# Performance work log

Measured on AMD Instinct MI355X. Metric: run time of the kernel, lower is better.

## Reference

```python
import jax, jax.numpy as jnp
import numpy as np

D = 64       # hidden_dim
ED = 16      # edge_dim
N = 50000
E = 400000
T = 2
STEP = 0.5   # euler fixed step over t in [0,1] -> 2 steps
EPS = 1e-5

def setup_inputs() -> dict:
    key = jax.random.key(0)
    ks = jax.random.split(key, 14)
    def lin(k, fi, fo):
        return jax.random.normal(k, (fi, fo), jnp.float32) / np.sqrt(fi)
    return {
        'h_seq': jax.random.normal(ks[0], (T, N, D), jnp.float32),
        'edge_attr': jax.random.normal(ks[1], (T, E, ED), jnp.float32),
        # msg_net: MLP(2D+ED -> D -> D), 2 layers with ReLU
        'W1': lin(ks[2], 2 * D + ED, D), 'b1': jnp.zeros((D,), jnp.float32),
        'W2': lin(ks[3], D, D),          'b2': jnp.zeros((D,), jnp.float32),
        # dynamics_net: Linear(2D,D) -> LayerNorm -> SiLU -> Linear(D,D) -> Tanh
        'Wd1': lin(ks[4], 2 * D, D), 'bd1': jnp.zeros((D,), jnp.float32),
        'ln_g': jnp.ones((D,), jnp.float32), 'ln_b': jnp.zeros((D,), jnp.float32),
        'Wd2': lin(ks[5], D, D), 'bd2': jnp.zeros((D,), jnp.float32),
        'edge_index': jax.random.randint(ks[6], (T, 2, E), 0, N, jnp.int32),
    }

def _ode_func(h, row, col, ea, W1, b1, W2, b2, Wd1, bd1, ln_g, ln_b, Wd2, bd2):
    # identity transport: Q_uv @ h_v == h_v
    h_transported = h[col]                              # [E, D]
    msg_in = jnp.concatenate([h[row], h_transported, ea], axis=-1)  # [E, 2D+ED]
    msg = jax.nn.relu(msg_in @ W1 + b1) @ W2 + b2       # [E, D]
    agg = jax.ops.segment_sum(msg, row, num_segments=h.shape[0])    # [N, D]
    x = jnp.concatenate([h, agg], axis=-1) @ Wd1 + bd1  # [N, D]
    mu = x.mean(-1, keepdims=True)
    var = x.var(-1, keepdims=True)
    x = (x - mu) * jax.lax.rsqrt(var + EPS) * ln_g + ln_b
    x = jax.nn.silu(x) @ Wd2 + bd2
    return jnp.tanh(x)

def reference(h_seq, edge_attr, W1, b1, W2, b2, Wd1, bd1, ln_g, ln_b, Wd2, bd2, edge_index):
    params = (W1, b1, W2, b2, Wd1, bd1, ln_g, ln_b, Wd2, bd2)
    n_steps = int(round(1.0 / STEP))
    h_prev = h_seq[0]
    disagreements = []
    for t in range(T):
        row, col = edge_index[t, 0], edge_index[t, 1]
        ea = edge_attr[t]
        h = h_prev + h_seq[t]                           # h_fused
        for _ in range(n_steps):                        # fixed-step Euler
            h = h + STEP * _ode_func(h, row, col, ea, *params)
        diff = h[row] - h[col]                          # Q=I -> h_u - h_v
        disagreements.append(jnp.minimum((diff * diff).sum(-1), 1e4))
        h_prev = h
    return h_prev, jnp.stack(disagreements)             # h_final [N,D], D [T,E]
```

## Files before the change

### kernel.cpp

```cpp
#include <hip/hip_runtime.h>

#define NN 50000
#define EE 400000
#define NT64 6250
#define EGRID 1250
#define NBLK 782
#define SBLK 49

typedef __bf16 bf16x8 __attribute__((ext_vector_type(8)));
typedef float f32x4 __attribute__((ext_vector_type(4)));

static __device__ __forceinline__ ushort f2bf(float f) {
    union { float f; unsigned int i; } x; x.f = f;
    unsigned int r = x.i + 0x7fffu + ((x.i >> 16) & 1u);
    return (ushort)(r >> 16);
}
static __device__ __forceinline__ float bf2f(ushort u) {
    union { unsigned int i; float f; } x; x.i = ((unsigned int)u) << 16; return x.f;
}
static __device__ __forceinline__ unsigned pack2(float lo, float hi) {
    return (unsigned)f2bf(lo) | ((unsigned)f2bf(hi) << 16);
}
static __device__ __forceinline__ float fast_tanh(float x) {
    float e = __expf(2.f * x);
    return 1.f - 2.f / (e + 1.f);
}
static __device__ __forceinline__ bf16x8 pk8(float4 f0, float4 f1) {
    union { uint4 u; bf16x8 v; } z;
    z.u = make_uint4(pack2(f0.x, f0.y), pack2(f0.z, f0.w),
                     pack2(f1.x, f1.y), pack2(f1.z, f1.w));
    return z.v;
}
static __device__ __forceinline__ bf16x8 zero8() {
    union { uint4 u; bf16x8 v; } z;
    z.u = make_uint4(0u, 0u, 0u, 0u);
    return z.v;
}

__global__ __launch_bounds__(256) void prep_edge_k(
    const float* __restrict__ W1, const float* __restrict__ W2,
    const float* __restrict__ b1, const float* __restrict__ b2,
    ushort* __restrict__ B1P, ushort* __restrict__ B2P,
    float* __restrict__ b1f, float* __restrict__ b2f)
{
    int idx = blockIdx.x * 256 + threadIdx.x;
    if (idx < 10240) {
        int j = idx & 7, n = (idx >> 3) & 63, qk = idx >> 9;
        int kc = qk >> 2, quad = qk & 3;
        int k = kc * 32 + quad * 8 + j;
        B1P[idx] = (k < 144) ? f2bf(W1[k * 64 + n]) : (ushort)0;
    }
    if (idx < 4096) {
        int j = idx & 7, n = (idx >> 3) & 63, qk = idx >> 9;
        int kc = qk >> 2, quad = qk & 3;
        int k = kc * 32 + quad * 8 + j;
        B2P[idx] = f2bf(W2[k * 64 + n]);
    }
    if (idx < 64) { b1f[idx] = b1[idx]; b2f[idx] = b2[idx]; }
}

__global__ __launch_bounds__(256) void prep_node_k(
    const float* __restrict__ Wd1, const float* __restrict__ Wd2,
    const float* __restrict__ bd1, const float* __restrict__ lng,
    const float* __restrict__ lnb, const float* __restrict__ bd2,
    ushort* __restrict__ Wd1P, ushort* __restrict__ Wd2P,
    float* __restrict__ bd1f, float* __restrict__ lngf,
    float* __restrict__ lnbf, float* __restrict__ bd2f)
{
    int idx = blockIdx.x * 256 + threadIdx.x;
    if (idx < 8192) {
        int j = idx & 7, n = (idx >> 3) & 63, qk = idx >> 9;
        int kc = qk >> 2, quad = qk & 3;
        int k = kc * 32 + quad * 8 + j;
        Wd1P[idx] = f2bf(Wd1[k * 64 + n]);
    }
    if (idx < 4096) {
        int j = idx & 7, n = (idx >> 3) & 63, qk = idx >> 9;
        int kc = qk >> 2, quad = qk & 3;
        int k = kc * 32 + quad * 8 + j;
        Wd2P[idx] = f2bf(Wd2[k * 64 + n]);
    }
    if (idx < 64) {
        bd1f[idx] = bd1[idx]; lngf[idx] = lng[idx];
        lnbf[idx] = lnb[idx]; bd2f[idx] = bd2[idx];
    }
}

__global__ __launch_bounds__(256) void state_k(
    float* __restrict__ h, ushort* __restrict__ hb,
    const float* __restrict__ hseq_t, int mode)
{
    int i = blockIdx.x * 256 + threadIdx.x;
    float v = hseq_t[i];
    float r = (mode == 0) ? (2.f * v) : (h[i] + v);
    h[i] = r; hb[i] = f2bf(r);
}

__global__ __launch_bounds__(256) void zero_k(int* __restrict__ p, int n) {
    int i = blockIdx.x * 256 + threadIdx.x;
    if (i < n) p[i] = 0;
}
__global__ __launch_bounds__(256) void zero_f(float* __restrict__ p) {
    int i = blockIdx.x * 256 + threadIdx.x;
    p[i] = 0.f;
}
__global__ __launch_bounds__(256) void hist_k(const int* __restrict__ rows, int* __restrict__ counts) {
    int e = blockIdx.x * 256 + threadIdx.x;
    if (e < EE) atomicAdd(&counts[rows[e]], 1);
}

__global__ __launch_bounds__(256) void scanA_k(
    const int* __restrict__ counts, int* __restrict__ offsets, int* __restrict__ bsum)
{
    __shared__ int wsum[4];
    int tid = threadIdx.x, lane = tid & 63, w = tid >> 6;
    int i4 = blockIdx.x * 1024 + tid * 4;
    int4 v = make_int4(0, 0, 0, 0);
    if (i4 + 3 < NN) v = *(const int4*)(counts + i4);
    else {
        if (i4 < NN) v.x = counts[i4];
        if (i4 + 1 < NN) v.y = counts[i4 + 1];
        if (i4 + 2 < NN) v.z = counts[i4 + 2];
    }
    int s = v.x + v.y + v.z + v.w;
    int x = s;
    for (int off = 1; off < 64; off <<= 1) {
        int y = __shfl_up(x, off);
        if (lane >= off) x += y;
    }
    if (lane == 63) wsum[w] = x;
    __syncthreads();
    int wpre = 0;
    for (int j = 0; j < w; j++) wpre += wsum[j];
    int excl = wpre + x - s;
    int e0 = excl, e1 = e0 + v.x, e2 = e1 + v.y, e3 = e2 + v.z;
    if (i4 + 3 < NN) *(int4*)(offsets + i4) = make_int4(e0, e1, e2, e3);
    else {
        if (i4 < NN) offsets[i4] = e0;
        if (i4 + 1 < NN) offsets[i4 + 1] = e1;
        if (i4 + 2 < NN) offsets[i4 + 2] = e2;
    }
    if (tid == 255) bsum[blockIdx.x] = wpre + x;
}
__global__ __launch_bounds__(256) void scanC_k(
    int* __restrict__ offsets, const int* __restrict__ bsum, int* __restrict__ cursor)
{
    int i = blockIdx.x * 256 + threadIdx.x;
    if (i < NN) {
        int b = i >> 10;
        int add = 0;
        for (int j = 0; j < b; j++) add += bsum[j];
        int o = offsets[i] + add;
        offsets[i] = o; cursor[i] = o;
    }
    if (i == 0) offsets[NN] = EE;
}

__global__ __launch_bounds__(256) void fill_idx_k(
    const int* __restrict__ rows, int* __restrict__ cursor, int* __restrict__ esort)
{
    int e = blockIdx.x * 256 + threadIdx.x;
    if (e < EE) {
        int p = atomicAdd(&cursor[rows[e]], 1);
        if ((unsigned)p < (unsigned)EE) esort[p] = e;
    }
}

__global__ __launch_bounds__(256) void gather_k(
    const int* __restrict__ esort, const int* __restrict__ rows,
    const int* __restrict__ cols, const float* __restrict__ ea,
    int* __restrict__ rsort, int* __restrict__ csort, ushort* __restrict__ eab)
{
    int p = blockIdx.x * 256 + threadIdx.x;
    if (p < EE) {
        int e = esort[p];
        rsort[p] = rows[e];
        csort[p] = cols[e];
        const float* sp = ea + (size_t)e * 16;
        float4 f0 = ((const float4*)sp)[0], f1 = ((const float4*)sp)[1];
        float4 f2 = ((const float4*)sp)[2], f3 = ((const float4*)sp)[3];
        uint4* dp = (uint4*)(eab + (size_t)p * 16);
        dp[0] = make_uint4(pack2(f0.x, f0.y), pack2(f0.z, f0.w),
                           pack2(f1.x, f1.y), pack2(f1.z, f1.w));
        dp[1] = make_uint4(pack2(f2.x, f2.y), pack2(f2.z, f2.w),
                           pack2(f3.x, f3.y), pack2(f3.z, f3.w));
    }
}

__global__ __launch_bounds__(256, 5) void edge_k(
    const ushort* __restrict__ hb,
    const int* __restrict__ ridx, const int* __restrict__ cidx,
    const ushort* __restrict__ eab,
    const ushort* __restrict__ B1P, const ushort* __restrict__ B2P,
    const float* __restrict__ b1f, const float* __restrict__ b2f,
    ushort* __restrict__ msg)
{
    __shared__ __attribute__((aligned(16))) ushort sB1[10240];
    __shared__ __attribute__((aligned(16))) ushort sH[64 * 72];

    int tid = threadIdx.x;
    int lane = tid & 63, wave = tid >> 6;
    int m = lane & 15, quad = lane >> 4;

    for (int i = tid; i < 10240 / 8; i += 256) ((uint4*)sB1)[i] = ((const uint4*)B1P)[i];
    bf16x8 b2r[2][4];
    for (int kc = 0; kc < 2; kc++)
        for (int nt = 0; nt < 4; nt++)
            b2r[kc][nt] = *(const bf16x8*)(B2P + ((kc * 4 + quad) * 64 + nt * 16 + m) * 8);
    float b1v[4], b2v[4];
    for (int nt = 0; nt < 4; nt++) { b1v[nt] = b1f[nt * 16 + m]; b2v[nt] = b2f[nt * 16 + m]; }
    __syncthreads();

    ushort* sHw = sH + wave * 1152;
    int sl = wave * 16 + m;
    int t0 = blockIdx.x * 5;
    int r_n = ridx[t0 * 64 + sl], c_n = cidx[t0 * 64 + sl];

    for (int t = t0; t < t0 + 5; t++) {
        int s = t * 64 + sl;
        int r = r_n, c = c_n;

        bf16x8 a[5];
        a[0] = *(const bf16x8*)(hb + (size_t)r * 64 + quad * 8);
        a[1] = *(const bf16x8*)(hb + (size_t)r * 64 + 32 + quad * 8);
        a[2] = *(const bf16x8*)(hb + (size_t)c * 64 + quad * 8);
        a[3] = *(const bf16x8*)(hb + (size_t)c * 64 + 32 + quad * 8);
        a[4] = zero8();
        if (quad < 2) a[4] = *(const bf16x8*)(eab + (size_t)s * 16 + quad * 8);

        int tn = t + 1; if (tn >= t0 + 5) tn = t;
        int sn = tn * 64 + sl;
        r_n = ridx[sn]; c_n = cidx[sn];

        f32x4 acc[4];
        #pragma unroll
        for (int nt = 0; nt < 4; nt++) acc[nt] = (f32x4){0.f, 0.f, 0.f, 0.f};
        #pragma unroll
        for (int kc = 0; kc < 5; kc++) {
            #pragma unroll
            for (int nt = 0; nt < 4; nt++) {
                bf16x8 b = *(const bf16x8*)(sB1 + ((kc * 4 + quad) * 64 + nt * 16 + m) * 8);
                acc[nt] = __builtin_amdgcn_mfma_f32_16x16x32_bf16(a[kc], b, acc[nt], 0, 0, 0);
            }
        }

        __builtin_amdgcn_wave_barrier();
        #pragma unroll
        for (int nt = 0; nt < 4; nt++) {
            int colid = nt * 16 + m;
            float bb = b1v[nt];
            #pragma unroll
            for (int rr = 0; rr < 4; rr++) {
                float v = acc[nt][rr] + bb;
                v = v > 0.f ? v : 0.f;
                sHw[(quad * 4 + rr) * 72 + colid] = f2bf(v);
            }
        }
        __builtin_amdgcn_wave_barrier();

        f32x4 acc2[4];
        #pragma unroll
        for (int nt = 0; nt < 4; nt++) acc2[nt] = (f32x4){0.f, 0.f, 0.f, 0.f};
        #pragma unroll
        for (int kc = 0; kc < 2; kc++) {
            bf16x8 av = *(const bf16x8*)(sHw + m * 72 + kc * 32 + quad * 8);
            #pragma unroll
            for (int nt = 0; nt < 4; nt++) {
                acc2[nt] = __builtin_amdgcn_mfma_f32_16x16x32_bf16(av, b2r[kc][nt], acc2[nt], 0, 0, 0);
            }
        }

        #pragma unroll
        for (int nt = 0; nt < 4; nt++) {
            int colid = nt * 16 + m;
            float bb = b2v[nt];
            #pragma unroll
            for (int rr = 0; rr < 4; rr++) {
                int so = t * 64 + wave * 16 + quad * 4 + rr;
                msg[(size_t)so * 64 + colid] = f2bf(acc2[nt][rr] + bb);
            }
        }
    }
}

__global__ __launch_bounds__(256, 5) void nodeagg_k(
    float* __restrict__ h, ushort* __restrict__ hbm,
    const ushort* __restrict__ msg, const int* __restrict__ offsets,
    const ushort* __restrict__ Wd1P, const ushort* __restrict__ Wd2P,
    const float* __restrict__ bd1f, const float* __restrict__ lngf,
    const float* __restrict__ lnbf, const float* __restrict__ bd2f)
{
    __shared__ __attribute__((aligned(16))) float aggL[64][68];
    __shared__ __attribute__((aligned(16))) ushort sX[64 * 72];
    int tid = threadIdx.x;
    int lane = tid & 63, wave = tid >> 6;
    int m = lane & 15, quad = lane >> 4;
    int nbase = blockIdx.x * 64;

    for (int idx = wave; idx < 64; idx += 4) {
        int n = nbase + idx;
        float a = 0.f;
        if (n < NN) {
            int bgn = offsets[n], end2 = offsets[n + 1];
            int i = bgn;
            for (; i + 4 <= end2; i += 4) {
                a += bf2f(msg[(size_t)i * 64 + lane]);
                a += bf2f(msg[(size_t)(i + 1) * 64 + lane]);
                a += bf2f(msg[(size_t)(i + 2) * 64 + lane]);
                a += bf2f(msg[(size_t)(i + 3) * 64 + lane]);
            }
            for (; i < end2; i++) a += bf2f(msg[(size_t)i * 64 + lane]);
        }
        aggL[idx][lane] = a;
    }

    float gA[4], bA[4], d1[4], d2[4];
    for (int nt = 0; nt < 4; nt++) {
        int f = nt * 16 + m;
        d1[nt] = bd1f[f]; gA[nt] = lngf[f]; bA[nt] = lnbf[f]; d2[nt] = bd2f[f];
    }
    __syncthreads();

    int n_true = nbase + wave * 16 + m;
    bool own = (n_true < NN);
    int n = own ? n_true : (NN - 1);
    int nl = wave * 16 + m;
    bf16x8 A[4];
    A[0] = *(const bf16x8*)(hbm + (size_t)n * 64 + quad * 8);
    A[1] = *(const bf16x8*)(hbm + (size_t)n * 64 + 32 + quad * 8);
    {
        float4 g0 = *(const float4*)&aggL[nl][quad * 8];
        float4 g1 = *(const float4*)&aggL[nl][quad * 8 + 4];
        float4 g2 = *(const float4*)&aggL[nl][32 + quad * 8];
        float4 g3 = *(const float4*)&aggL[nl][32 + quad * 8 + 4];
        A[2] = pk8(g0, g1);
        A[3] = pk8(g2, g3);
    }

    f32x4 acc[4];
    #pragma unroll
    for (int nt = 0; nt < 4; nt++) acc[nt] = (f32x4){0.f, 0.f, 0.f, 0.f};
    #pragma unroll
    for (int kc = 0; kc < 4; kc++) {
        #pragma unroll
        for (int nt = 0; nt < 4; nt++) {
            bf16x8 b = *(const bf16x8*)(Wd1P + ((kc * 4 + quad) * 64 + nt * 16 + m) * 8);
            acc[nt] = __builtin_amdgcn_mfma_f32_16x16x32_bf16(A[kc], b, acc[nt], 0, 0, 0);
        }
    }

    float xs[4][4];
    #pragma unroll
    for (int nt = 0; nt < 4; nt++)
        #pragma unroll
        for (int r = 0; r < 4; r++)
            xs[nt][r] = acc[nt][r] + d1[nt];

    ushort* sXw = sX + wave * 1152;
    #pragma unroll
    for (int r = 0; r < 4; r++) {
        float s1 = 0.f, s2 = 0.f;
        #pragma unroll
        for (int nt = 0; nt < 4; nt++) { float v = xs[nt][r]; s1 += v; s2 += v * v; }
        for (int off = 1; off < 16; off <<= 1) {
            s1 += __shfl_xor(s1, off);
            s2 += __shfl_xor(s2, off);
        }
        float mean = s1 * (1.f / 64.f);
        float var = fmaxf(s2 * (1.f / 64.f) - mean * mean, 0.f);
        float rstd = rsqrtf(var + 1e-5f);
        #pragma unroll
        for (int nt = 0; nt < 4; nt++) {
            float xn = (xs[nt][r] - mean) * rstd * gA[nt] + bA[nt];
            float slv = xn / (1.f + __expf(-xn));
            sXw[(quad * 4 + r) * 72 + nt * 16 + m] = f2bf(slv);
        }
    }
    __builtin_amdgcn_wave_barrier();

    f32x4 acc2[4];
    #pragma unroll
    for (int nt = 0; nt < 4; nt++) acc2[nt] = (f32x4){0.f, 0.f, 0.f, 0.f};
    #pragma unroll
    for (int kc = 0; kc < 2; kc++) {
        bf16x8 av = *(const bf16x8*)(sXw + m * 72 + kc * 32 + quad * 8);
        #pragma unroll
        for (int nt = 0; nt < 4; nt++) {
            bf16x8 b = *(const bf16x8*)(Wd2P + ((kc * 4 + quad) * 64 + nt * 16 + m) * 8);
            acc2[nt] = __builtin_amdgcn_mfma_f32_16x16x32_bf16(av, b, acc2[nt], 0, 0, 0);
        }
    }

    #pragma unroll
    for (int r = 0; r < 4; r++) {
        int g = nbase + wave * 16 + quad * 4 + r;
        if (g < NN) {
            #pragma unroll
            for (int nt = 0; nt < 4; nt++) {
                int f = nt * 16 + m;
                float y = fast_tanh(acc2[nt][r] + d2[nt]);
                float hn = h[(size_t)g * 64 + f] + 0.5f * y;
                h[(size_t)g * 64 + f] = hn;
                hbm[(size_t)g * 64 + f] = f2bf(hn);
            }
        }
    }
}

__global__ __launch_bounds__(256, 5) void edge_fb_k(
    const ushort* __restrict__ hb,
    const int* __restrict__ ridx, const int* __restrict__ cidx,
    const float* __restrict__ eaf,
    const ushort* __restrict__ B1P, const ushort* __restrict__ B2P,
    const float* __restrict__ b1f, const float* __restrict__ b2f,
    float* __restrict__ agg)
{
    __shared__ __attribute__((aligned(16))) ushort sB1[10240];
    __shared__ __attribute__((aligned(16))) ushort sH[64 * 72];

    int tid = threadIdx.x;
    int lane = tid & 63, wave = tid >> 6;
    int m = lane & 15, quad = lane >> 4;

    for (int i = tid; i < 10240 / 8; i += 256) ((uint4*)sB1)[i] = ((const uint4*)B1P)[i];
    bf16x8 b2r[2][4];
    for (int kc = 0; kc < 2; kc++)
        for (int nt = 0; nt < 4; nt++)
            b2r[kc][nt] = *(const bf16x8*)(B2P + ((kc * 4 + quad) * 64 + nt * 16 + m) * 8);
    float b1v[4], b2v[4];
    for (int nt = 0; nt < 4; nt++) { b1v[nt] = b1f[nt * 16 + m]; b2v[nt] = b2f[nt * 16 + m]; }
    __syncthreads();

    ushort* sHw = sH + wave * 1152;
    int sl = wave * 16 + m;
    int t0 = blockIdx.x * 5;

    for (int t = t0; t < t0 + 5; t++) {
        int s = t * 64 + sl;
        int r = ridx[s], c = cidx[s];
        bf16x8 a[5];
        a[0] = *(const bf16x8*)(hb + (size_t)r * 64 + quad * 8);
        a[1] = *(const bf16x8*)(hb + (size_t)r * 64 + 32 + quad * 8);
        a[2] = *(const bf16x8*)(hb + (size_t)c * 64 + quad * 8);
        a[3] = *(const bf16x8*)(hb + (size_t)c * 64 + 32 + quad * 8);
        a[4] = zero8();
        if (quad < 2) {
            const float* sp = eaf + (size_t)s * 16 + quad * 8;
            a[4] = pk8(((const float4*)sp)[0], ((const float4*)sp)[1]);
        }
        f32x4 acc[4];
        #pragma unroll
        for (int nt = 0; nt < 4; nt++) acc[nt] = (f32x4){0.f, 0.f, 0.f, 0.f};
        #pragma unroll
        for (int kc = 0; kc < 5; kc++)
            #pragma unroll
            for (int nt = 0; nt < 4; nt++) {
                bf16x8 b = *(const bf16x8*)(sB1 + ((kc * 4 + quad) * 64 + nt * 16 + m) * 8);
                acc[nt] = __builtin_amdgcn_mfma_f32_16x16x32_bf16(a[kc], b, acc[nt], 0, 0, 0);
            }
        __builtin_amdgcn_wave_barrier();
        #pragma unroll
        for (int nt = 0; nt < 4; nt++) {
            float bb = b1v[nt];
            #pragma unroll
            for (int rr = 0; rr < 4; rr++) {
                float v = acc[nt][rr] + bb;
                v = v > 0.f ? v : 0.f;
                sHw[(quad * 4 + rr) * 72 + nt * 16 + m] = f2bf(v);
            }
        }
        __builtin_amdgcn_wave_barrier();
        f32x4 acc2[4];
        #pragma unroll
        for (int nt = 0; nt < 4; nt++) acc2[nt] = (f32x4){0.f, 0.f, 0.f, 0.f};
        #pragma unroll
        for (int kc = 0; kc < 2; kc++) {
            bf16x8 av = *(const bf16x8*)(sHw + m * 72 + kc * 32 + quad * 8);
            #pragma unroll
            for (int nt = 0; nt < 4; nt++)
                acc2[nt] = __builtin_amdgcn_mfma_f32_16x16x32_bf16(av, b2r[kc][nt], acc2[nt], 0, 0, 0);
        }
        int base = t * 64 + wave * 16 + quad * 4;
        int r0 = ridx[base], r1 = ridx[base + 1], r2 = ridx[base + 2], r3 = ridx[base + 3];
        #pragma unroll
        for (int nt = 0; nt < 4; nt++) {
            int colid = nt * 16 + m;
            float bb = b2v[nt];
            float v0 = acc2[nt][0] + bb, v1 = acc2[nt][1] + bb;
            float v2 = acc2[nt][2] + bb, v3 = acc2[nt][3] + bb;
            float sum = v0; int pr = r0;
            if (r1 == pr) sum += v1;
            else { atomicAdd(&agg[(size_t)pr * 64 + colid], sum); pr = r1; sum = v1; }
            if (r2 == pr) sum += v2;
            else { atomicAdd(&agg[(size_t)pr * 64 + colid], sum); pr = r2; sum = v2; }
            if (r3 == pr) sum += v3;
            else { atomicAdd(&agg[(size_t)pr * 64 + colid], sum); pr = r3; sum = v3; }
            atomicAdd(&agg[(size_t)pr * 64 + colid], sum);
        }
    }
}

__global__ __launch_bounds__(256, 4) void node_k(
    float* __restrict__ h, ushort* __restrict__ hbm,
    float* __restrict__ agg,
    const ushort* __restrict__ Wd1P, const ushort* __restrict__ Wd2P,
    const float* __restrict__ bd1f, const float* __restrict__ lngf,
    const float* __restrict__ lnbf, const float* __restrict__ bd2f)
{
    __shared__ __attribute__((aligned(16))) ushort sB1[8192];
    __shared__ __attribute__((aligned(16))) ushort sB2[4096];
    __shared__ __attribute__((aligned(16))) ushort sX[64 * 72];
    int tid = threadIdx.x;
    int lane = tid & 63, wave = tid >> 6;
    int m = lane & 15, quad = lane >> 4;
    int nbase = blockIdx.x * 64;

    for (int i = tid; i < 8192 / 8; i += 256) ((uint4*)sB1)[i] = ((const uint4*)Wd1P)[i];
    for (int i = tid; i < 4096 / 8; i += 256) ((uint4*)sB2)[i] = ((const uint4*)Wd2P)[i];
    float gA[4], bA[4], d1[4], d2[4];
    for (int nt = 0; nt < 4; nt++) {
        int f = nt * 16 + m;
        d1[nt] = bd1f[f]; gA[nt] = lngf[f]; bA[nt] = lnbf[f]; d2[nt] = bd2f[f];
    }
    __syncthreads();

    int n_true = nbase + wave * 16 + m;
    bool own = (n_true < NN);
    int n = own ? n_true : (NN - 1);
    bf16x8 A[4];
    A[0] = *(const bf16x8*)(hbm + (size_t)n * 64 + quad * 8);
    A[1] = *(const bf16x8*)(hbm + (size_t)n * 64 + 32 + quad * 8);
    {
        const float* ap = agg + (size_t)n * 64 + quad * 8;
        float4 g0 = ((const float4*)ap)[0], g1 = ((const float4*)ap)[1];
        const float* ap2 = agg + (size_t)n * 64 + 32 + quad * 8;
        float4 g2 = ((const float4*)ap2)[0], g3 = ((const float4*)ap2)[1];
        A[2] = pk8(g0, g1);
        A[3] = pk8(g2, g3);
        if (own) {
            float4 z = make_float4(0.f, 0.f, 0.f, 0.f);
            ((float4*)(agg + (size_t)n * 64 + quad * 8))[0] = z;
            ((float4*)(agg + (size_t)n * 64 + quad * 8))[1] = z;
            ((float4*)(agg + (size_t)n * 64 + 32 + quad * 8))[0] = z;
            ((float4*)(agg + (size_t)n * 64 + 32 + quad * 8))[1] = z;
        }
    }

    f32x4 acc[4];
    #pragma unroll
    for (int nt = 0; nt < 4; nt++) acc[nt] = (f32x4){0.f, 0.f, 0.f, 0.f};
    #pragma unroll
    for (int kc = 0; kc < 4; kc++)
        #pragma unroll
        for (int nt = 0; nt < 4; nt++) {
            bf16x8 b = *(const bf16x8*)(sB1 + ((kc * 4 + quad) * 64 + nt * 16 + m) * 8);
            acc[nt] = __builtin_amdgcn_mfma_f32_16x16x32_bf16(A[kc], b, acc[nt], 0, 0, 0);
        }

    float xs[4][4];
    #pragma unroll
    for (int nt = 0; nt < 4; nt++)
        #pragma unroll
        for (int r = 0; r < 4; r++)
            xs[nt][r] = acc[nt][r] + d1[nt];

    ushort* sXw = sX + wave * 1152;
    #pragma unroll
    for (int r = 0; r < 4; r++) {
        float s1 = 0.f, s2 = 0.f;
        #pragma unroll
        for (int nt = 0; nt < 4; nt++) { float v = xs[nt][r]; s1 += v; s2 += v * v; }
        for (int off = 1; off < 16; off <<= 1) {
            s1 += __shfl_xor(s1, off);
            s2 += __shfl_xor(s2, off);
        }
        float mean = s1 * (1.f / 64.f);
        float var = fmaxf(s2 * (1.f / 64.f) - mean * mean, 0.f);
        float rstd = rsqrtf(var + 1e-5f);
        #pragma unroll
        for (int nt = 0; nt < 4; nt++) {
            float xn = (xs[nt][r] - mean) * rstd * gA[nt] + bA[nt];
            float slv = xn / (1.f + __expf(-xn));
            sXw[(quad * 4 + r) * 72 + nt * 16 + m] = f2bf(slv);
        }
    }
    __builtin_amdgcn_wave_barrier();

    f32x4 acc2[4];
    #pragma unroll
    for (int nt = 0; nt < 4; nt++) acc2[nt] = (f32x4){0.f, 0.f, 0.f, 0.f};
    #pragma unroll
    for (int kc = 0; kc < 2; kc++) {
        bf16x8 av = *(const bf16x8*)(sXw + m * 72 + kc * 32 + quad * 8);
        #pragma unroll
        for (int nt = 0; nt < 4; nt++) {
            bf16x8 b = *(const bf16x8*)(sB2 + ((kc * 4 + quad) * 64 + nt * 16 + m) * 8);
            acc2[nt] = __builtin_amdgcn_mfma_f32_16x16x32_bf16(av, b, acc2[nt], 0, 0, 0);
        }
    }

    #pragma unroll
    for (int r = 0; r < 4; r++) {
        int g = nbase + wave * 16 + quad * 4 + r;
        if (g < NN) {
            #pragma unroll
            for (int nt = 0; nt < 4; nt++) {
                int f = nt * 16 + m;
                float y = fast_tanh(acc2[nt][r] + d2[nt]);
                float hn = h[(size_t)g * 64 + f] + 0.5f * y;
                h[(size_t)g * 64 + f] = hn;
                hbm[(size_t)g * 64 + f] = f2bf(hn);
            }
        }
    }
}

__global__ __launch_bounds__(256) void dis_k(
    const float* __restrict__ h, const int* __restrict__ rows,
    const int* __restrict__ cols, float* __restrict__ outp)
{
    int tid = threadIdx.x;
    int e = blockIdx.x * 16 + (tid >> 4);
    int l16 = tid & 15;
    int r = rows[e], c = cols[e];
    float4 a = *(const float4*)(h + (size_t)r * 64 + l16 * 4);
    float4 b = *(const float4*)(h + (size_t)c * 64 + l16 * 4);
    float dx = a.x - b.x, dy = a.y - b.y, dz = a.z - b.z, dw = a.w - b.w;
    float s = dx * dx + dy * dy + dz * dz + dw * dw;
    for (int off = 1; off < 16; off <<= 1) s += __shfl_xor(s, off);
    if (l16 == 0) outp[e] = (s < 1e4f ? s : 1e4f);
}

__global__ __launch_bounds__(256) void final_k(const float* __restrict__ h, float* __restrict__ out) {
    int i = blockIdx.x * 256 + threadIdx.x;
    out[i] = h[i];
}

extern "C" void kernel_launch(void* const* d_in, const int* in_sizes, int n_in,
                              void* d_out, int out_size, void* d_ws, size_t ws_size,
                              hipStream_t stream) {
    const float* h_seq = (const float*)d_in[0];
    const float* eattr = (const float*)d_in[1];
    const float* W1 = (const float*)d_in[2];
    const float* b1 = (const float*)d_in[3];
    const float* W2 = (const float*)d_in[4];
    const float* b2 = (const float*)d_in[5];
    const float* Wd1 = (const float*)d_in[6];
    const float* bd1 = (const float*)d_in[7];
    const float* lng = (const float*)d_in[8];
    const float* lnb = (const float*)d_in[9];
    const float* Wd2 = (const float*)d_in[10];
    const float* bd2 = (const float*)d_in[11];
    const int* ei = (const int*)d_in[12];
    float* out = (float*)d_out;

    char* wsp = (char*)d_ws;
    size_t used = 0;
    auto carve = [&](size_t b) {
        void* p = (void*)(wsp + used);
        used += (b + 255) & ~(size_t)255;
        return p;
    };
    float* h0     = (float*)carve((size_t)NN * 64 * 4);
    ushort* hb0   = (ushort*)carve((size_t)NN * 64 * 2);
    float* agg    = (float*)carve((size_t)NN * 64 * 4);
    ushort* B1P   = (ushort*)carve(10240 * 2);
    ushort* B2P   = (ushort*)carve(4096 * 2);
    ushort* Wd1P  = (ushort*)carve(8192 * 2);
    ushort* Wd2P  = (ushort*)carve(4096 * 2);
    float* b1f    = (float*)carve(256);
    float* b2f    = (float*)carve(256);
    float* bd1f   = (float*)carve(256);
    float* lngf   = (float*)carve(256);
    float* lnbf   = (float*)carve(256);
    float* bd2f   = (float*)carve(256);
    int* counts   = (int*)carve((size_t)NN * 4);
    int* offsets  = (int*)carve((size_t)(NN + 1) * 4);
    int* cursor   = (int*)carve((size_t)NN * 4);
    int* bsum     = (int*)carve(256);
    int* esort    = (int*)carve((size_t)EE * 4);
    int* rsort    = (int*)carve((size_t)EE * 4);
    int* csort    = (int*)carve((size_t)EE * 4);
    ushort* eab   = (ushort*)carve((size_t)EE * 16 * 2);
    ushort* msg   = (ushort*)carve((size_t)EE * 64 * 2);
    const bool full = (used <= ws_size);

    prep_edge_k<<<40, 256, 0, stream>>>(W1, W2, b1, b2, B1P, B2P, b1f, b2f);
    prep_node_k<<<32, 256, 0, stream>>>(Wd1, Wd2, bd1, lng, lnb, bd2, Wd1P, Wd2P, bd1f, lngf, lnbf, bd2f);
    if (!full) zero_f<<<12500, 256, 0, stream>>>(agg);

    for (int t = 0; t < 2; t++) {
        const int* rows = ei + (size_t)t * 2 * EE;
        const int* cols = rows + EE;
        const float* eat = eattr + (size_t)t * EE * 16;
        state_k<<<12500, 256, 0, stream>>>(h0, hb0, h_seq + (size_t)t * NN * 64, t);
        if (full) {
            zero_k<<<196, 256, 0, stream>>>(counts, NN);
            hist_k<<<1563, 256, 0, stream>>>(rows, counts);
            scanA_k<<<SBLK, 256, 0, stream>>>(counts, offsets, bsum);
            scanC_k<<<196, 256, 0, stream>>>(offsets, bsum, cursor);
            fill_idx_k<<<1563, 256, 0, stream>>>(rows, cursor, esort);
            gather_k<<<1563, 256, 0, stream>>>(esort, rows, cols, eat, rsort, csort, eab);
            for (int s = 0; s < 2; s++) {
                edge_k<<<EGRID, 256, 0, stream>>>(hb0, rsort, csort, eab,
                                                  B1P, B2P, b1f, b2f, msg);
                nodeagg_k<<<NBLK, 256, 0, stream>>>(h0, hb0, msg, offsets, Wd1P, Wd2P,
                                                    bd1f, lngf, lnbf, bd2f);
            }
        } else {
            for (int s = 0; s < 2; s++) {
                edge_fb_k<<<EGRID, 256, 0, stream>>>(hb0, rows, cols, eat,
                                                     B1P, B2P, b1f, b2f, agg);
                node_k<<<NBLK, 256, 0, stream>>>(h0, hb0, agg, Wd1P, Wd2P,
                                                 bd1f, lngf, lnbf, bd2f);
            }
        }
        dis_k<<<25000, 256, 0, stream>>>(h0, rows, cols, out + (size_t)NN * 64 + (size_t)t * EE);
    }
    final_k<<<12500, 256, 0, stream>>>(h0, out);
}
```

Measured before the change: 564.0 us.

## Restructure edge kernel to one tile per block, fuse final copy, sort-ordered dis_k

The edge kernel now processes one 64-edge tile per block with XCD-aware tile remapping, reads W1/W2 fragments directly from global memory instead of staging them in LDS, and raises launch bounds to allow more waves. The node aggregation kernel assigns contiguous nodes per wave, uses two accumulators, replaces the block sync with a wave barrier, and writes the final h directly to the output, which removes the separate copy kernel. The disagreement kernel reads sorted row/col indices for better locality and scatters through the permutation. The risks are more global/L2 traffic for weights and scattered output writes in dis_k.

```diff
diff --git a/kernel.cpp b/kernel.cpp
--- a/kernel.cpp
+++ b/kernel.cpp
@@ -187,7 +187,7 @@
     }
 }
 
-__global__ __launch_bounds__(256, 5) void edge_k(
+__global__ __launch_bounds__(256, 8) void edge_k(
     const ushort* __restrict__ hb,
     const int* __restrict__ ridx, const int* __restrict__ cidx,
     const ushort* __restrict__ eab,
@@ -195,100 +195,90 @@
     const float* __restrict__ b1f, const float* __restrict__ b2f,
     ushort* __restrict__ msg)
 {
-    __shared__ __attribute__((aligned(16))) ushort sB1[10240];
     __shared__ __attribute__((aligned(16))) ushort sH[64 * 72];
 
     int tid = threadIdx.x;
     int lane = tid & 63, wave = tid >> 6;
     int m = lane & 15, quad = lane >> 4;
 
-    for (int i = tid; i < 10240 / 8; i += 256) ((uint4*)sB1)[i] = ((const uint4*)B1P)[i];
-    bf16x8 b2r[2][4];
-    for (int kc = 0; kc < 2; kc++)
-        for (int nt = 0; nt < 4; nt++)
-            b2r[kc][nt] = *(const bf16x8*)(B2P + ((kc * 4 + quad) * 64 + nt * 16 + m) * 8);
+    int bid = blockIdx.x;
+    int xcd = bid & 7, ii = bid >> 3;
+    int t = (xcd < 2) ? xcd * 782 + ii : 1564 + (xcd - 2) * 781 + ii;
+
+    int sl = wave * 16 + m;
+    int s = t * 64 + sl;
+    int r = ridx[s], c = cidx[s];
+
     float b1v[4], b2v[4];
+    #pragma unroll
     for (int nt = 0; nt < 4; nt++) { b1v[nt] = b1f[nt * 16 + m]; b2v[nt] = b2f[nt * 16 + m]; }
-    __syncthreads();
+
+    bf16x8 a[5];
+    a[0] = *(const bf16x8*)(hb + (size_t)r * 64 + quad * 8);
+    a[1] = *(const bf16x8*)(hb + (size_t)r * 64 + 32 + quad * 8);
+    a[2] = *(const bf16x8*)(hb + (size_t)c * 64 + quad * 8);
+    a[3] = *(const bf16x8*)(hb + (size_t)c * 64 + 32 + quad * 8);
+    a[4] = zero8();
+    if (quad < 2) a[4] = *(const bf16x8*)(eab + (size_t)s * 16 + quad * 8);
+
+    f32x4 acc[4];
+    #pragma unroll
+    for (int nt = 0; nt < 4; nt++) acc[nt] = (f32x4){0.f, 0.f, 0.f, 0.f};
+    #pragma unroll
+    for (int kc = 0; kc < 5; kc++) {
+        #pragma unroll
+        for (int nt = 0; nt < 4; nt++) {
+            bf16x8 b = *(const bf16x8*)(B1P + ((kc * 4 + quad) * 64 + nt * 16 + m) * 8);
+            acc[nt] = __builtin_amdgcn_mfma_f32_16x16x32_bf16(a[kc], b, acc[nt], 0, 0, 0);
+        }
+    }
 
     ushort* sHw = sH + wave * 1152;
-    int sl = wave * 16 + m;
-    int t0 = blockIdx.x * 5;
-    int r_n = ridx[t0 * 64 + sl], c_n = cidx[t0 * 64 + sl];
-
-    for (int t = t0; t < t0 + 5; t++) {
-        int s = t * 64 + sl;
-        int r = r_n, c = c_n;
-
-        bf16x8 a[5];
-        a[0] = *(const bf16x8*)(hb + (size_t)r * 64 + quad * 8);
-        a[1] = *(const bf16x8*)(hb + (size_t)r * 64 + 32 + quad * 8);
-        a[2] = *(const bf16x8*)(hb + (size_t)c * 64 + quad * 8);
-        a[3] = *(const bf16x8*)(hb + (size_t)c * 64 + 32 + quad * 8);
-        a[4] = zero8();
-        if (quad < 2) a[4] = *(const bf16x8*)(eab + (size_t)s * 16 + quad * 8);
-
-        int tn = t + 1; if (tn >= t0 + 5) tn = t;
-        int sn = tn * 64 + sl;
-        r_n = ridx[sn]; c_n = cidx[sn];
-
-        f32x4 acc[4];
-        #pragma unroll
-        for (int nt = 0; nt < 4; nt++) acc[nt] = (f32x4){0.f, 0.f, 0.f, 0.f};
-        #pragma unroll
-        for (int kc = 0; kc < 5; kc++) {
-            #pragma unroll
-            for (int nt = 0; nt < 4; nt++) {
-                bf16x8 b = *(const bf16x8*)(sB1 + ((kc * 4 + quad) * 64 + nt * 16 + m) * 8);
-                acc[nt] = __builtin_amdgcn_mfma_f32_16x16x32_bf16(a[kc], b, acc[nt], 0, 0, 0);
-            }
-        }
-
-        __builtin_amdgcn_wave_barrier();
-        #pragma unroll
-        for (int nt = 0; nt < 4; nt++) {
-            int colid = nt * 16 + m;
-            float bb = b1v[nt];
-            #pragma unroll
-            for (int rr = 0; rr < 4; rr++) {
-                float v = acc[nt][rr] + bb;
-                v = v > 0.f ? v : 0.f;
-                sHw[(quad * 4 + rr) * 72 + colid] = f2bf(v);
-            }
-        }
-        __builtin_amdgcn_wave_barrier();
-
-        f32x4 acc2[4];
-        #pragma unroll
-        for (int nt = 0; nt < 4; nt++) acc2[nt] = (f32x4){0.f, 0.f, 0.f, 0.f};
-        #pragma unroll
-        for (int kc = 0; kc < 2; kc++) {
-            bf16x8 av = *(const bf16x8*)(sHw + m * 72 + kc * 32 + quad * 8);
-            #pragma unroll
-            for (int nt = 0; nt < 4; nt++) {
-                acc2[nt] = __builtin_amdgcn_mfma_f32_16x16x32_bf16(av, b2r[kc][nt], acc2[nt], 0, 0, 0);
-            }
-        }
-
-        #pragma unroll
-        for (int nt = 0; nt < 4; nt++) {
-            int colid = nt * 16 + m;
-            float bb = b2v[nt];
-            #pragma unroll
-            for (int rr = 0; rr < 4; rr++) {
-                int so = t * 64 + wave * 16 + quad * 4 + rr;
-                msg[(size_t)so * 64 + colid] = f2bf(acc2[nt][rr] + bb);
-            }
-        }
-    }
-}
-
-__global__ __launch_bounds__(256, 5) void nodeagg_k(
+    #pragma unroll
+    for (int nt = 0; nt < 4; nt++) {
+        int colid = nt * 16 + m;
+        float bb = b1v[nt];
+        #pragma unroll
+        for (int rr = 0; rr < 4; rr++) {
+            float v = acc[nt][rr] + bb;
+            v = v > 0.f ? v : 0.f;
+            sHw[(quad * 4 + rr) * 72 + colid] = f2bf(v);
+        }
+    }
+    __builtin_amdgcn_wave_barrier();
+
+    f32x4 acc2[4];
+    #pragma unroll
+    for (int nt = 0; nt < 4; nt++) acc2[nt] = (f32x4){0.f, 0.f, 0.f, 0.f};
+    #pragma unroll
+    for (int kc = 0; kc < 2; kc++) {
+        bf16x8 av = *(const bf16x8*)(sHw + m * 72 + kc * 32 + quad * 8);
+        #pragma unroll
+        for (int nt = 0; nt < 4; nt++) {
+            bf16x8 b = *(const bf16x8*)(B2P + ((kc * 4 + quad) * 64 + nt * 16 + m) * 8);
+            acc2[nt] = __builtin_amdgcn_mfma_f32_16x16x32_bf16(av, b, acc2[nt], 0, 0, 0);
+        }
+    }
+
+    #pragma unroll
+    for (int nt = 0; nt < 4; nt++) {
+        int colid = nt * 16 + m;
+        float bb = b2v[nt];
+        #pragma unroll
+        for (int rr = 0; rr < 4; rr++) {
+            int so = t * 64 + wave * 16 + quad * 4 + rr;
+            msg[(size_t)so * 64 + colid] = f2bf(acc2[nt][rr] + bb);
+        }
+    }
+}
+
+__global__ __launch_bounds__(256, 6) void nodeagg_k(
     float* __restrict__ h, ushort* __restrict__ hbm,
     const ushort* __restrict__ msg, const int* __restrict__ offsets,
     const ushort* __restrict__ Wd1P, const ushort* __restrict__ Wd2P,
     const float* __restrict__ bd1f, const float* __restrict__ lngf,
-    const float* __restrict__ lnbf, const float* __restrict__ bd2f)
+    const float* __restrict__ lnbf, const float* __restrict__ bd2f,
+    float* __restrict__ outF)
 {
     __shared__ __attribute__((aligned(16))) float aggL[64][68];
     __shared__ __attribute__((aligned(16))) ushort sX[64 * 72];
@@ -297,29 +287,30 @@
     int m = lane & 15, quad = lane >> 4;
     int nbase = blockIdx.x * 64;
 
-    for (int idx = wave; idx < 64; idx += 4) {
+    for (int idx = wave * 16; idx < wave * 16 + 16; idx++) {
         int n = nbase + idx;
-        float a = 0.f;
+        float a0 = 0.f, a1 = 0.f;
         if (n < NN) {
             int bgn = offsets[n], end2 = offsets[n + 1];
             int i = bgn;
             for (; i + 4 <= end2; i += 4) {
-                a += bf2f(msg[(size_t)i * 64 + lane]);
-                a += bf2f(msg[(size_t)(i + 1) * 64 + lane]);
-                a += bf2f(msg[(size_t)(i + 2) * 64 + lane]);
-                a += bf2f(msg[(size_t)(i + 3) * 64 + lane]);
+                a0 += bf2f(msg[(size_t)i * 64 + lane]);
+                a1 += bf2f(msg[(size_t)(i + 1) * 64 + lane]);
+                a0 += bf2f(msg[(size_t)(i + 2) * 64 + lane]);
+                a1 += bf2f(msg[(size_t)(i + 3) * 64 + lane]);
             }
-            for (; i < end2; i++) a += bf2f(msg[(size_t)i * 64 + lane]);
-        }
-        aggL[idx][lane] = a;
+            for (; i < end2; i++) a0 += bf2f(msg[(size_t)i * 64 + lane]);
+        }
+        aggL[idx][lane] = a0 + a1;
     }
 
     float gA[4], bA[4], d1[4], d2[4];
+    #pragma unroll
     for (int nt = 0; nt < 4; nt++) {
         int f = nt * 16 + m;
         d1[nt] = bd1f[f]; gA[nt] = lngf[f]; bA[nt] = lnbf[f]; d2[nt] = bd2f[f];
     }
-    __syncthreads();
+    __builtin_amdgcn_wave_barrier();
 
     int n_true = nbase + wave * 16 + m;
     bool own = (n_true < NN);
@@ -402,6 +393,7 @@
                 float hn = h[(size_t)g * 64 + f] + 0.5f * y;
                 h[(size_t)g * 64 + f] = hn;
                 hbm[(size_t)g * 64 + f] = f2bf(hn);
+                if (outF) outF[(size_t)g * 64 + f] = hn;
             }
         }
     }
@@ -616,13 +608,15 @@
 }
 
 __global__ __launch_bounds__(256) void dis_k(
-    const float* __restrict__ h, const int* __restrict__ rows,
-    const int* __restrict__ cols, float* __restrict__ outp)
+    const float* __restrict__ h, const int* __restrict__ ridx,
+    const int* __restrict__ cidx, const int* __restrict__ emap,
+    float* __restrict__ outp)
 {
     int tid = threadIdx.x;
-    int e = blockIdx.x * 16 + (tid >> 4);
+    int p = blockIdx.x * 16 + (tid >> 4);
     int l16 = tid & 15;
-    int r = rows[e], c = cols[e];
+    int r = ridx[p], c = cidx[p];
+    int e = emap ? emap[p] : p;
     float4 a = *(const float4*)(h + (size_t)r * 64 + l16 * 4);
     float4 b = *(const float4*)(h + (size_t)c * 64 + l16 * 4);
     float dx = a.x - b.x, dy = a.y - b.y, dz = a.z - b.z, dw = a.w - b.w;
@@ -702,11 +696,14 @@
             fill_idx_k<<<1563, 256, 0, stream>>>(rows, cursor, esort);
             gather_k<<<1563, 256, 0, stream>>>(esort, rows, cols, eat, rsort, csort, eab);
             for (int s = 0; s < 2; s++) {
-                edge_k<<<EGRID, 256, 0, stream>>>(hb0, rsort, csort, eab,
-                                                  B1P, B2P, b1f, b2f, msg);
+                edge_k<<<NT64, 256, 0, stream>>>(hb0, rsort, csort, eab,
+                                                 B1P, B2P, b1f, b2f, msg);
+                float* outF = (t == 1 && s == 1) ? out : (float*)0;
                 nodeagg_k<<<NBLK, 256, 0, stream>>>(h0, hb0, msg, offsets, Wd1P, Wd2P,
-                                                    bd1f, lngf, lnbf, bd2f);
+                                                    bd1f, lngf, lnbf, bd2f, outF);
             }
+            dis_k<<<25000, 256, 0, stream>>>(h0, rsort, csort, esort,
+                                             out + (size_t)NN * 64 + (size_t)t * EE);
         } else {
             for (int s = 0; s < 2; s++) {
                 edge_fb_k<<<EGRID, 256, 0, stream>>>(hb0, rows, cols, eat,
@@ -714,8 +711,9 @@
                 node_k<<<NBLK, 256, 0, stream>>>(h0, hb0, agg, Wd1P, Wd2P,
                                                  bd1f, lngf, lnbf, bd2f);
             }
-        }
-        dis_k<<<25000, 256, 0, stream>>>(h0, rows, cols, out + (size_t)NN * 64 + (size_t)t * EE);
-    }
-    final_k<<<12500, 256, 0, stream>>>(h0, out);
-}
+            dis_k<<<25000, 256, 0, stream>>>(h0, rows, cols, (const int*)0,
+                                             out + (size_t)NN * 64 + (size_t)t * EE);
+            if (t == 1) final_k<<<12500, 256, 0, stream>>>(h0, out);
+        }
+    }
+}
```

Result: slower. 625.1 us (+10.8%).
